# Optimization experiments

Measured on AMD Instinct MI355X. Metric: run time of the kernel, lower is better.

The kernel has to match this reference:

```python
import jax, jax.numpy as jnp
import numpy as np

N, E = 100000, 1000000          # nodes, edges
IN, OUT = 64, 64                # feature dims
R, B = 16, 8                    # num_rels, num_bases


def setup_inputs() -> dict:
    key = jax.random.key(0)
    k = jax.random.split(key, 6)
    h = jax.random.normal(k[0], (N, IN), jnp.float32)
    weight = jax.random.normal(k[1], (B, IN, OUT), jnp.float32) * 0.05
    w_comp = jax.random.normal(k[2], (R, B), jnp.float32) * 0.3
    src = jax.random.randint(k[3], (E,), 0, N, jnp.int32)
    dst = jax.random.randint(k[4], (E,), 0, N, jnp.int32)
    rel = jax.random.randint(k[5], (E,), 0, R, jnp.int32)
    return {"h": h, "weight": weight, "w_comp": w_comp,
            "src": src, "dst": dst, "rel": rel}


def _rel_weights(weight, w_comp):
    # Faithful replication of the torch basis-combination including its
    # exact (reinterpreting) view calls:
    #   weight.view(in, B, out); matmul(w_comp, .); .view(R, in, out)
    V = weight.reshape(IN, B, OUT)                 # reinterpret, not transpose
    M = jnp.einsum('rb,ibo->iro', w_comp, V)       # [IN, R, OUT]
    return M.reshape(R, IN, OUT)


def reference(h, weight, w_comp, src, dst, rel):
    W = _rel_weights(weight, w_comp)               # [R, IN, OUT]
    # msg_e = h[src_e] @ W[rel_e]; computed without materializing [E,IN,OUT]:
    proj = jnp.einsum('nd,rdf->nrf', h, W)         # [N, R, OUT]
    msg = proj[src, rel]                           # [E, OUT] per-edge gather
    h2 = jax.ops.segment_sum(msg, dst, num_segments=N)  # fn.sum -> 'h2'
    # apply_func: bias is None (falsy); returns activation(old h).
    # Note: original apply_func reads but does not use h2 (tutorial quirk);
    # we return both the updated 'h' and the aggregated 'h2'.
    h_new = jax.nn.relu(h)
    return h_new, h2
```

## Files before the change

### kernel.cpp

```cpp
#include <hip/hip_runtime.h>
#include <hip/hip_bf16.h>

#define NN 100000
#define EE 1000000
#define FDIM 64
#define NREL 16
#define NBASE 8
#define HN (NN * FDIM)
#define H4 (HN / 4)
#define WSZ (NREL * FDIM * FDIM)
#define GX 96

__global__ void zero_counts_kernel(int* counts) {
    if (threadIdx.x < NREL) counts[threadIdx.x] = 0;
}

__global__ void compute_w_kernel(const float* __restrict__ weight,
                                 const float* __restrict__ w_comp,
                                 float* __restrict__ W) {
    int q = blockIdx.x * blockDim.x + threadIdx.x;
    if (q >= WSZ) return;
    int i = q >> 10;
    int r = (q >> 6) & 15;
    int o = q & 63;
    float acc = 0.f;
#pragma unroll
    for (int b = 0; b < NBASE; ++b)
        acc = fmaf(w_comp[r * NBASE + b], weight[i * 512 + b * 64 + o], acc);
    W[q] = acc;
}

__global__ void relu_zero_kernel(const float4* __restrict__ h4,
                                 float4* __restrict__ out4) {
    int i = blockIdx.x * blockDim.x + threadIdx.x;
    if (i < H4) {
        float4 v = h4[i];
        v.x = fmaxf(v.x, 0.f); v.y = fmaxf(v.y, 0.f);
        v.z = fmaxf(v.z, 0.f); v.w = fmaxf(v.w, 0.f);
        out4[i] = v;
        out4[H4 + i] = make_float4(0.f, 0.f, 0.f, 0.f);
    }
}

__global__ void hist_kernel(const int* __restrict__ rel, int* __restrict__ counts) {
    __shared__ int lc[NREL];
    if (threadIdx.x < NREL) lc[threadIdx.x] = 0;
    __syncthreads();
    int stride = gridDim.x * blockDim.x;
    for (int i = blockIdx.x * blockDim.x + threadIdx.x; i < EE; i += stride)
        atomicAdd(&lc[rel[i]], 1);
    __syncthreads();
    if (threadIdx.x < NREL && lc[threadIdx.x] > 0)
        atomicAdd(&counts[threadIdx.x], lc[threadIdx.x]);
}

__global__ void scan_kernel(const int* __restrict__ counts,
                            int* __restrict__ offsets, int* __restrict__ cursors) {
    if (threadIdx.x == 0 && blockIdx.x == 0) {
        int acc = 0;
        for (int r = 0; r < NREL; ++r) { offsets[r] = acc; cursors[r] = acc; acc += counts[r]; }
        offsets[NREL] = acc;
    }
}

__global__ void scatter_kernel(const int* __restrict__ rel, const int* __restrict__ src,
                               const int* __restrict__ dst, int* __restrict__ cursors,
                               int* __restrict__ src_bin, int* __restrict__ dst_bin) {
    __shared__ int lhist[NREL];
    __shared__ int lbase[NREL];
    int i = blockIdx.x * blockDim.x + threadIdx.x;
    if (threadIdx.x < NREL) lhist[threadIdx.x] = 0;
    __syncthreads();
    int r = 0, rank = 0;
    if (i < EE) { r = rel[i]; rank = atomicAdd(&lhist[r], 1); }
    __syncthreads();
    if (threadIdx.x < NREL && lhist[threadIdx.x] > 0)
        lbase[threadIdx.x] = atomicAdd(&cursors[threadIdx.x], lhist[threadIdx.x]);
    __syncthreads();
    if (i < EE) {
        int pos = lbase[r] + rank;
        src_bin[pos] = src[i];
        dst_bin[pos] = dst[i];
    }
}

__global__ __launch_bounds__(256) void edge_kernel(
    const int* __restrict__ offsets, const int* __restrict__ src_bin,
    const int* __restrict__ dst_bin, const float* __restrict__ h,
    const float* __restrict__ W, float* __restrict__ h2) {
    const int rel = blockIdx.y;
    const int lane = threadIdx.x & 63;
    const int start = offsets[rel];
    const int end = offsets[rel + 1];

    float wcol[FDIM];
    const float* wbase = W + rel * 4096 + lane;
#pragma unroll
    for (int d = 0; d < FDIM; ++d) wcol[d] = wbase[d * 64];

    const int nw = GX * 4;
    const int wave = blockIdx.x * 4 + (threadIdx.x >> 6);
    const int cnt = end - start;
    const int per = (cnt + nw - 1) / nw;
    int i0 = start + wave * per;
    int i1 = i0 + per; if (i1 > end) i1 = end;

    for (int i = i0; i < i1; ++i) {
        int s  = __builtin_amdgcn_readfirstlane(src_bin[i]);
        int dv = __builtin_amdgcn_readfirstlane(dst_bin[i]);
        const float* __restrict__ hrow = h + (size_t)s * FDIM;
        float a0 = 0.f, a1 = 0.f, a2 = 0.f, a3 = 0.f;
#pragma unroll
        for (int d = 0; d < FDIM; d += 4) {
            a0 = fmaf(hrow[d],     wcol[d],     a0);
            a1 = fmaf(hrow[d + 1], wcol[d + 1], a1);
            a2 = fmaf(hrow[d + 2], wcol[d + 2], a2);
            a3 = fmaf(hrow[d + 3], wcol[d + 3], a3);
        }
        float acc = (a0 + a1) + (a2 + a3);
        unsafeAtomicAdd(&h2[(size_t)dv * FDIM + lane], acc);
    }
}

extern "C" void kernel_launch(void* const* d_in, const int* in_sizes, int n_in,
                              void* d_out, int out_size, void* d_ws, size_t ws_size,
                              hipStream_t stream) {
    const float* h      = (const float*)d_in[0];
    const float* weight = (const float*)d_in[1];
    const float* w_comp = (const float*)d_in[2];
    const int*   src    = (const int*)d_in[3];
    const int*   dst    = (const int*)d_in[4];
    const int*   rel    = (const int*)d_in[5];

    float* out_hnew = (float*)d_out;
    float* out_h2   = out_hnew + HN;

    float* W       = (float*)d_ws;
    int*   meta    = (int*)((char*)d_ws + WSZ * 4);
    int*   counts  = meta;
    int*   offsets = meta + 16;
    int*   cursors = meta + 33;
    int*   src_bin = (int*)((char*)d_ws + WSZ * 4 + 256);
    int*   dst_bin = src_bin + EE;

    hipLaunchKernelGGL(zero_counts_kernel, dim3(1), dim3(64), 0, stream, counts);
    hipLaunchKernelGGL(compute_w_kernel, dim3(WSZ / 256), dim3(256), 0, stream,
                       weight, w_comp, W);
    hipLaunchKernelGGL(relu_zero_kernel, dim3((H4 + 255) / 256), dim3(256), 0, stream,
                       (const float4*)h, (float4*)out_hnew);
    hipLaunchKernelGGL(hist_kernel, dim3(1024), dim3(256), 0, stream, rel, counts);
    hipLaunchKernelGGL(scan_kernel, dim3(1), dim3(64), 0, stream, counts, offsets, cursors);
    hipLaunchKernelGGL(scatter_kernel, dim3((EE + 255) / 256), dim3(256), 0, stream,
                       rel, src, dst, cursors, src_bin, dst_bin);
    hipLaunchKernelGGL(edge_kernel, dim3(GX, NREL), dim3(256), 0, stream,
                       offsets, src_bin, dst_bin, h, W, out_h2);
}
```

Baseline: 392.3 us.

## Bucket edges by destination and fuse aggregation with bf16 MFMA projection

After: 608.4 us. 55.1% more time.

```diff
diff --git a/kernel.cpp b/kernel.cpp
--- a/kernel.cpp
+++ b/kernel.cpp
@@ -9,117 +9,133 @@
 #define HN (NN * FDIM)
 #define H4 (HN / 4)
 #define WSZ (NREL * FDIM * FDIM)
-#define GX 96
+#define NBIN 6250
+#define KDIM 1024
 
-__global__ void zero_counts_kernel(int* counts) {
-    if (threadIdx.x < NREL) counts[threadIdx.x] = 0;
+typedef __attribute__((ext_vector_type(8))) short short8;
+typedef __attribute__((ext_vector_type(4))) float f32x4;
+
+static __device__ __forceinline__ ushort f2bf(float f) {
+    __hip_bfloat16 b = __float2bfloat16(f);
+    return *(ushort*)&b;
 }
 
-__global__ void compute_w_kernel(const float* __restrict__ weight,
-                                 const float* __restrict__ w_comp,
-                                 float* __restrict__ W) {
-    int q = blockIdx.x * blockDim.x + threadIdx.x;
-    if (q >= WSZ) return;
-    int i = q >> 10;
-    int r = (q >> 6) & 15;
-    int o = q & 63;
-    float acc = 0.f;
+__global__ void prep_kernel(const float4* __restrict__ h4, float4* __restrict__ out4,
+                            const float* __restrict__ weight,
+                            const float* __restrict__ w_comp,
+                            ushort* __restrict__ WT2, int* __restrict__ cnt) {
+    int gid = blockIdx.x * 256 + threadIdx.x;
+    if (gid < NBIN + 8) cnt[gid] = 0;
+    if (gid < WSZ) {
+        int o = gid >> 10;
+        int k = gid & 1023;
+        int r = k >> 6;
+        int d = k & 63;
+        const float* wc = w_comp + (d & 15) * NBASE;
+        const float* wv = weight + (size_t)(4 * r + (d >> 4)) * 512 + o;
+        float acc = 0.f;
 #pragma unroll
-    for (int b = 0; b < NBASE; ++b)
-        acc = fmaf(w_comp[r * NBASE + b], weight[i * 512 + b * 64 + o], acc);
-    W[q] = acc;
-}
-
-__global__ void relu_zero_kernel(const float4* __restrict__ h4,
-                                 float4* __restrict__ out4) {
-    int i = blockIdx.x * blockDim.x + threadIdx.x;
-    if (i < H4) {
-        float4 v = h4[i];
+        for (int b = 0; b < NBASE; ++b)
+            acc = fmaf(wc[b], wv[b * 64], acc);
+        WT2[gid] = f2bf(acc);
+    }
+    if (gid < H4) {
+        float4 v = h4[gid];
         v.x = fmaxf(v.x, 0.f); v.y = fmaxf(v.y, 0.f);
         v.z = fmaxf(v.z, 0.f); v.w = fmaxf(v.w, 0.f);
-        out4[i] = v;
-        out4[H4 + i] = make_float4(0.f, 0.f, 0.f, 0.f);
+        out4[gid] = v;
     }
 }
 
-__global__ void hist_kernel(const int* __restrict__ rel, int* __restrict__ counts) {
-    __shared__ int lc[NREL];
-    if (threadIdx.x < NREL) lc[threadIdx.x] = 0;
-    __syncthreads();
+__global__ void hist_kernel(const int* __restrict__ dst, int* __restrict__ cnt) {
     int stride = gridDim.x * blockDim.x;
     for (int i = blockIdx.x * blockDim.x + threadIdx.x; i < EE; i += stride)
-        atomicAdd(&lc[rel[i]], 1);
-    __syncthreads();
-    if (threadIdx.x < NREL && lc[threadIdx.x] > 0)
-        atomicAdd(&counts[threadIdx.x], lc[threadIdx.x]);
+        atomicAdd(&cnt[dst[i] >> 4], 1);
 }
 
-__global__ void scan_kernel(const int* __restrict__ counts,
-                            int* __restrict__ offsets, int* __restrict__ cursors) {
-    if (threadIdx.x == 0 && blockIdx.x == 0) {
-        int acc = 0;
-        for (int r = 0; r < NREL; ++r) { offsets[r] = acc; cursors[r] = acc; acc += counts[r]; }
-        offsets[NREL] = acc;
+__global__ __launch_bounds__(1024) void scan_kernel(const int* __restrict__ cnt,
+                                                    int* __restrict__ off,
+                                                    int* __restrict__ cur) {
+    __shared__ int lds[1024];
+    int t = threadIdx.x;
+    int lo = t * 7, hi = lo + 7;
+    if (lo > NBIN) lo = NBIN;
+    if (hi > NBIN) hi = NBIN;
+    int s = 0;
+    for (int i = lo; i < hi; ++i) s += cnt[i];
+    lds[t] = s;
+    __syncthreads();
+    for (int o = 1; o < 1024; o <<= 1) {
+        int u = (t >= o) ? lds[t - o] : 0;
+        __syncthreads();
+        lds[t] += u;
+        __syncthreads();
+    }
+    int base = (t > 0) ? lds[t - 1] : 0;
+    for (int i = lo; i < hi; ++i) { off[i] = base; cur[i] = base; base += cnt[i]; }
+    if (t == 1023) off[NBIN] = lds[1023];
+}
+
+__global__ void scatter_kernel(const int* __restrict__ src, const int* __restrict__ dst,
+                               const int* __restrict__ rel, int* __restrict__ cur,
+                               int* __restrict__ pidx) {
+    int i = blockIdx.x * blockDim.x + threadIdx.x;
+    if (i < EE) {
+        int d = dst[i];
+        int pos = atomicAdd(&cur[d >> 4], 1);
+        pidx[pos] = (src[i] << 8) | (rel[i] << 4) | (d & 15);
     }
 }
 
-__global__ void scatter_kernel(const int* __restrict__ rel, const int* __restrict__ src,
-                               const int* __restrict__ dst, int* __restrict__ cursors,
-                               int* __restrict__ src_bin, int* __restrict__ dst_bin) {
-    __shared__ int lhist[NREL];
-    __shared__ int lbase[NREL];
-    int i = blockIdx.x * blockDim.x + threadIdx.x;
-    if (threadIdx.x < NREL) lhist[threadIdx.x] = 0;
+__global__ __launch_bounds__(256) void rgcn_fused_kernel(
+    const int* __restrict__ off, const int* __restrict__ pidx,
+    const float* __restrict__ h, const ushort* __restrict__ WT2,
+    float* __restrict__ h2) {
+    __shared__ float S[16 * KDIM];
+    const int tid = threadIdx.x;
+    const int lane = tid & 63;
+    const int wvid = tid >> 6;
+    for (int i = tid; i < 16 * KDIM; i += 256) S[i] = 0.f;
     __syncthreads();
-    int r = 0, rank = 0;
-    if (i < EE) { r = rel[i]; rank = atomicAdd(&lhist[r], 1); }
+
+    const int b = blockIdx.x;
+    const int s = off[b], e = off[b + 1];
+
+#pragma unroll 4
+    for (int i = s + wvid; i < e; i += 4) {
+        int p  = __builtin_amdgcn_readfirstlane(pidx[i]);
+        int sn = p >> 8;
+        int ld = p & 15;
+        int k  = (((p >> 4) & 15) << 6) + lane;
+        float v = h[(size_t)sn * FDIM + lane];
+        int idx = ld * KDIM + (k ^ ((ld & 7) << 2));
+        __hip_atomic_fetch_add(&S[idx], v, __ATOMIC_RELAXED, __HIP_MEMORY_SCOPE_WORKGROUP);
+    }
     __syncthreads();
-    if (threadIdx.x < NREL && lhist[threadIdx.x] > 0)
-        lbase[threadIdx.x] = atomicAdd(&cursors[threadIdx.x], lhist[threadIdx.x]);
-    __syncthreads();
-    if (i < EE) {
-        int pos = lbase[r] + rank;
-        src_bin[pos] = src[i];
-        dst_bin[pos] = dst[i];
+
+    const int quad = lane >> 4, l15 = lane & 15;
+    const int C = (l15 & 7) << 2;
+    const float4* S4 = (const float4*)S;
+    const short8* wrow = (const short8*)(WT2 + (size_t)(wvid * 16 + l15) * KDIM);
+    f32x4 acc = (f32x4){0.f, 0.f, 0.f, 0.f};
+#pragma unroll
+    for (int ks = 0; ks < 32; ++ks) {
+        int k0 = ks * 32 + quad * 8;
+        float4 a = S4[l15 * 256 + ((k0 ^ C) >> 2)];
+        float4 c = S4[l15 * 256 + (((k0 + 4) ^ C) >> 2)];
+        short8 Afr;
+        Afr[0] = (short)f2bf(a.x); Afr[1] = (short)f2bf(a.y);
+        Afr[2] = (short)f2bf(a.z); Afr[3] = (short)f2bf(a.w);
+        Afr[4] = (short)f2bf(c.x); Afr[5] = (short)f2bf(c.y);
+        Afr[6] = (short)f2bf(c.z); Afr[7] = (short)f2bf(c.w);
+        short8 Bfr = wrow[ks * 4 + quad];
+        acc = __builtin_amdgcn_mfma_f32_16x16x32_bf16(Afr, Bfr, acc, 0, 0, 0);
     }
-}
-
-__global__ __launch_bounds__(256) void edge_kernel(
-    const int* __restrict__ offsets, const int* __restrict__ src_bin,
-    const int* __restrict__ dst_bin, const float* __restrict__ h,
-    const float* __restrict__ W, float* __restrict__ h2) {
-    const int rel = blockIdx.y;
-    const int lane = threadIdx.x & 63;
-    const int start = offsets[rel];
-    const int end = offsets[rel + 1];
-
-    float wcol[FDIM];
-    const float* wbase = W + rel * 4096 + lane;
+    const int v0 = b * 16;
+    const int ocol = wvid * 16 + l15;
 #pragma unroll
-    for (int d = 0; d < FDIM; ++d) wcol[d] = wbase[d * 64];
-
-    const int nw = GX * 4;
-    const int wave = blockIdx.x * 4 + (threadIdx.x >> 6);
-    const int cnt = end - start;
-    const int per = (cnt + nw - 1) / nw;
-    int i0 = start + wave * per;
-    int i1 = i0 + per; if (i1 > end) i1 = end;
-
-    for (int i = i0; i < i1; ++i) {
-        int s  = __builtin_amdgcn_readfirstlane(src_bin[i]);
-        int dv = __builtin_amdgcn_readfirstlane(dst_bin[i]);
-        const float* __restrict__ hrow = h + (size_t)s * FDIM;
-        float a0 = 0.f, a1 = 0.f, a2 = 0.f, a3 = 0.f;
-#pragma unroll
-        for (int d = 0; d < FDIM; d += 4) {
-            a0 = fmaf(hrow[d],     wcol[d],     a0);
-            a1 = fmaf(hrow[d + 1], wcol[d + 1], a1);
-            a2 = fmaf(hrow[d + 2], wcol[d + 2], a2);
-            a3 = fmaf(hrow[d + 3], wcol[d + 3], a3);
-        }
-        float acc = (a0 + a1) + (a2 + a3);
-        unsafeAtomicAdd(&h2[(size_t)dv * FDIM + lane], acc);
-    }
+    for (int r = 0; r < 4; ++r)
+        h2[(size_t)(v0 + quad * 4 + r) * FDIM + ocol] = acc[r];
 }
 
 extern "C" void kernel_launch(void* const* d_in, const int* in_sizes, int n_in,
@@ -135,23 +151,19 @@
     float* out_hnew = (float*)d_out;
     float* out_h2   = out_hnew + HN;
 
-    float* W       = (float*)d_ws;
-    int*   meta    = (int*)((char*)d_ws + WSZ * 4);
-    int*   counts  = meta;
-    int*   offsets = meta + 16;
-    int*   cursors = meta + 33;
-    int*   src_bin = (int*)((char*)d_ws + WSZ * 4 + 256);
-    int*   dst_bin = src_bin + EE;
+    char* ws = (char*)d_ws;
+    ushort* WT2  = (ushort*)ws;
+    int*    cnt  = (int*)(ws + 131072);
+    int*    off  = (int*)(ws + 156160);
+    int*    cur  = (int*)(ws + 181248);
+    int*    pidx = (int*)(ws + 206336);
 
-    hipLaunchKernelGGL(zero_counts_kernel, dim3(1), dim3(64), 0, stream, counts);
-    hipLaunchKernelGGL(compute_w_kernel, dim3(WSZ / 256), dim3(256), 0, stream,
-                       weight, w_comp, W);
-    hipLaunchKernelGGL(relu_zero_kernel, dim3((H4 + 255) / 256), dim3(256), 0, stream,
-                       (const float4*)h, (float4*)out_hnew);
-    hipLaunchKernelGGL(hist_kernel, dim3(1024), dim3(256), 0, stream, rel, counts);
-    hipLaunchKernelGGL(scan_kernel, dim3(1), dim3(64), 0, stream, counts, offsets, cursors);
+    hipLaunchKernelGGL(prep_kernel, dim3((H4 + 255) / 256), dim3(256), 0, stream,
+                       (const float4*)h, (float4*)out_hnew, weight, w_comp, WT2, cnt);
+    hipLaunchKernelGGL(hist_kernel, dim3(1024), dim3(256), 0, stream, dst, cnt);
+    hipLaunchKernelGGL(scan_kernel, dim3(1), dim3(1024), 0, stream, cnt, off, cur);
     hipLaunchKernelGGL(scatter_kernel, dim3((EE + 255) / 256), dim3(256), 0, stream,
-                       rel, src, dst, cursors, src_bin, dst_bin);
-    hipLaunchKernelGGL(edge_kernel, dim3(GX, NREL), dim3(256), 0, stream,
-                       offsets, src_bin, dst_bin, h, W, out_h2);
+                       src, dst, rel, cur, pidx);
+    hipLaunchKernelGGL(rgcn_fused_kernel, dim3(NBIN), dim3(256), 0, stream,
+                       off, pidx, h, WT2, out_h2);
 }
```
